# Kernel optimization log

Measured on AMD Instinct MI355X. Metric: run time of the kernel, lower is better.

The kernel has to match this reference:

```python
import jax, jax.numpy as jnp
import numpy as np
import math

D_MODEL = 1024
N_HEADS = 16
HEAD_DIM = D_MODEL // N_HEADS
N_LEVELS = 4
B = 8
MAX_LEN = 1024
LN_EPS = 1e-5


def setup_inputs() -> dict:
    key = jax.random.key(0)
    ks = jax.random.split(key, 6)
    lengths = np.array([1024, 768, 512, 896, 640, 1024, 576, 704], dtype=np.int32)
    N = int(lengths.sum())  # 6144
    batch_offsets = jnp.asarray(np.concatenate([[0], np.cumsum(lengths)]).astype(np.int32))
    x = jax.random.normal(ks[0], (N, D_MODEL), jnp.float32)
    levels = jax.random.randint(ks[1], (N, 1), 0, N_LEVELS).astype(jnp.float32)
    coords = jax.random.uniform(ks[2], (N, 2), jnp.float32) * 64.0
    positions = jnp.concatenate([levels, coords], axis=-1)  # [N, 3] = (level, y, x)
    ln_gamma = jnp.ones((D_MODEL,), jnp.float32)
    ln_beta = jnp.zeros((D_MODEL,), jnp.float32)
    w_qkv = jax.random.normal(ks[3], (D_MODEL, 3 * D_MODEL), jnp.float32) / math.sqrt(D_MODEL)
    w_out = jax.random.normal(ks[4], (D_MODEL, D_MODEL), jnp.float32) / math.sqrt(D_MODEL)
    # learned per-level, per-head rotary frequencies for 2 spatial coords
    base = 10.0 ** (-2.0 * np.arange(HEAD_DIM // 2) / HEAD_DIM)  # rope_theta = 10.0
    rope_freqs = (jnp.asarray(base, jnp.float32)[None, None, :, None]
                  * (1.0 + 0.1 * jax.random.normal(ks[5], (N_LEVELS, N_HEADS, HEAD_DIM // 2, 2), jnp.float32)))
    return {"x": x, "positions": positions, "batch_offsets": batch_offsets,
            "ln_gamma": ln_gamma, "ln_beta": ln_beta, "w_qkv": w_qkv,
            "w_out": w_out, "rope_freqs": rope_freqs}


def _layernorm(x, g, b):
    mu = jnp.mean(x, axis=-1, keepdims=True)
    var = jnp.mean(jnp.square(x - mu), axis=-1, keepdims=True)
    return (x - mu) * jax.lax.rsqrt(var + LN_EPS) * g + b


def _forward(x, positions, batch_offsets, ln_gamma, ln_beta, w_qkv, w_out, rope_freqs):
    N = x.shape[0]
    residual = x
    h = _layernorm(x, ln_gamma, ln_beta)
    q, k, v = jnp.split(h @ w_qkv, 3, axis=-1)  # each [N, D]

    # ragged -> padded batch layout
    tok = jnp.arange(N)
    batch_ids = jnp.searchsorted(batch_offsets[1:], tok, side='right')  # [N]
    pos_in_seq = tok - batch_offsets[batch_ids]                         # [N]
    lengths = batch_offsets[1:] - batch_offsets[:-1]                    # [B]
    valid = jnp.arange(MAX_LEN)[None, :] < lengths[:, None]             # [B, L]

    def pad(t, fill=0.0):
        out = jnp.full((B, MAX_LEN) + t.shape[1:], fill, t.dtype)
        return out.at[batch_ids, pos_in_seq].set(t)

    qp = pad(q).reshape(B, MAX_LEN, N_HEADS, HEAD_DIM)
    kp = pad(k).reshape(B, MAX_LEN, N_HEADS, HEAD_DIM)
    vp = pad(v).reshape(B, MAX_LEN, N_HEADS, HEAD_DIM)
    posp = pad(positions, fill=1.0)  # padded positions filled with ones (as in torch code)

    # multilevel RoPE: per-level learned freqs over 2 spatial coords
    lvl = jnp.clip(posp[..., 0].astype(jnp.int32), 0, N_LEVELS - 1)  # [B, L]
    f = rope_freqs[lvl]                                              # [B, L, H, K, 2]
    ang = jnp.einsum('blhkc,blc->blhk', f, posp[..., 1:])            # [B, L, H, K]
    cos, sin = jnp.cos(ang), jnp.sin(ang)

    def rot(t):  # rotate consecutive pairs of head_dim
        t = t.reshape(B, MAX_LEN, N_HEADS, HEAD_DIM // 2, 2)
        a, b = t[..., 0], t[..., 1]
        return jnp.stack([a * cos - b * sin, a * sin + b * cos], axis=-1).reshape(
            B, MAX_LEN, N_HEADS, HEAD_DIM)

    qr, kr = rot(qp), rot(kp)

    # masked SDPA (padded keys excluded; padded query rows are dropped on un-pad)
    scale = 1.0 / math.sqrt(HEAD_DIM)
    scores = jnp.einsum('blhd,bmhd->bhlm', qr, kr) * scale
    scores = jnp.where(valid[:, None, None, :], scores, jnp.float32(-1e9))
    attn = jax.nn.softmax(scores, axis=-1)
    o = jnp.einsum('bhlm,bmhd->blhd', attn, vp).reshape(B, MAX_LEN, D_MODEL)

    o = o[batch_ids, pos_in_seq]  # back to packed [N, D]
    return o @ w_out + residual


def reference(x, positions, batch_offsets, ln_gamma, ln_beta, w_qkv, w_out, rope_freqs):
    return _forward(x, positions, batch_offsets, ln_gamma, ln_beta, w_qkv, w_out, rope_freqs)
```

## Files before the change

### kernel.cpp

```cpp
#include <hip/hip_runtime.h>


typedef float  f32x4  __attribute__((ext_vector_type(4)));
typedef __bf16 bf16x8 __attribute__((ext_vector_type(8)));
typedef __bf16 bf16x4 __attribute__((ext_vector_type(4)));
typedef short  s16x4  __attribute__((ext_vector_type(4)));
typedef short  s16x8  __attribute__((ext_vector_type(8)));
typedef unsigned short u16x4 __attribute__((ext_vector_type(4)));

typedef __attribute__((address_space(1))) void as1_void_t;
typedef __attribute__((address_space(3))) void as3_void_t;

static __device__ __forceinline__ unsigned short f2bf(float f) {
  unsigned int u = __float_as_uint(f);
  u += 0x7fffu + ((u >> 16) & 1u);
  return (unsigned short)(u >> 16);
}
static __device__ __forceinline__ float bf2f(unsigned short s) {
  return __uint_as_float(((unsigned int)s) << 16);
}

static __device__ __forceinline__ void gload_lds16(const void* g, void* l) {
  __builtin_amdgcn_global_load_lds((as1_void_t*)g, (as3_void_t*)l, 16, 0, 0);
}

static __device__ __forceinline__ f32x4 mfma32(bf16x8 a, bf16x8 b, f32x4 c) {
  return __builtin_amdgcn_mfma_f32_16x16x32_bf16(a, b, c, 0, 0, 0);
}
static __device__ __forceinline__ f32x4 mfma16(s16x4 a, s16x4 b, f32x4 c) {
  return __builtin_amdgcn_mfma_f32_16x16x16bf16_1k(a, b, c, 0, 0, 0);
}

__global__ __launch_bounds__(256) void ln_kernel(
    const float* __restrict__ x, const float* __restrict__ gamma,
    const float* __restrict__ beta, unsigned short* __restrict__ h, int Ntok) {
  int row  = blockIdx.x * 4 + (threadIdx.x >> 6);
  int lane = threadIdx.x & 63;
  const float* xr = x + (size_t)row * 1024;
  f32x4 v[4];
  float s = 0.f, ss = 0.f;
#pragma unroll
  for (int c = 0; c < 4; ++c) {
    v[c] = *(const f32x4*)(xr + c * 256 + lane * 4);
#pragma unroll
    for (int j = 0; j < 4; ++j) { s += v[c][j]; ss += v[c][j] * v[c][j]; }
  }
#pragma unroll
  for (int d = 1; d < 64; d <<= 1) {
    s  += __shfl_xor(s, d);
    ss += __shfl_xor(ss, d);
  }
  float mu  = s * (1.f / 1024.f);
  float var = ss * (1.f / 1024.f) - mu * mu;
  float inv = rsqrtf(var + 1e-5f);
#pragma unroll
  for (int c = 0; c < 4; ++c) {
    f32x4 gv = *(const f32x4*)(gamma + c * 256 + lane * 4);
    f32x4 bv = *(const f32x4*)(beta  + c * 256 + lane * 4);
    u16x4 hv;
#pragma unroll
    for (int j = 0; j < 4; ++j) hv[j] = f2bf((v[c][j] - mu) * inv * gv[j] + bv[j]);
    *(u16x4*)(h + (size_t)row * 1024 + c * 256 + lane * 4) = hv;
  }
}

__global__ __launch_bounds__(256) void transpose_bf16(
    const float* __restrict__ in, unsigned short* __restrict__ out, int R, int C) {
  __shared__ unsigned short tile[64][65];
  int c0 = blockIdx.x * 64, r0 = blockIdx.y * 64;
  int t = threadIdx.x;
  int tr = t >> 6, tc = t & 63;
#pragma unroll
  for (int i = 0; i < 16; ++i) {
    int rr = i * 4 + tr;
    tile[tc][rr] = f2bf(in[(size_t)(r0 + rr) * C + c0 + tc]);
  }
  __syncthreads();
#pragma unroll
  for (int i = 0; i < 16; ++i) {
    int cc = i * 4 + tr;
    out[(size_t)(c0 + cc) * R + r0 + tc] = tile[cc][tc];
  }
}

__global__ __launch_bounds__(256) void gemm_qkv(
    const unsigned short* __restrict__ A, const unsigned short* __restrict__ Bt,
    unsigned short* __restrict__ Cqkv, int M, int K) {
  __shared__ unsigned short Alds[128 * 32];
  __shared__ unsigned short Blds[128 * 32];
  int n0 = blockIdx.x * 128, m0 = blockIdx.y * 128;
  int t = threadIdx.x, lane = t & 63, wave = t >> 6;
  int wr = wave >> 1, wc = wave & 1;
  int r = lane & 15, g = lane >> 4;
  f32x4 acc[4][4] = {};

  int srow = lane >> 2;
  int scol = (lane & 3) * 8;

  for (int k0 = 0; k0 < K; k0 += 32) {
    __syncthreads();
#pragma unroll
    for (int c = 0; c < 2; ++c) {
      int seg = wave * 2 + c;
      gload_lds16(A  + (size_t)(m0 + seg * 16 + srow) * K + k0 + scol,
                  Alds + seg * 16 * 32);
      gload_lds16(Bt + (size_t)(n0 + seg * 16 + srow) * K + k0 + scol,
                  Blds + seg * 16 * 32);
    }
    __syncthreads();
    bf16x8 a[4], b[4];
#pragma unroll
    for (int m = 0; m < 4; ++m)
      a[m] = *(const bf16x8*)(Alds + (wr * 64 + m * 16 + r) * 32 + g * 8);
#pragma unroll
    for (int n = 0; n < 4; ++n)
      b[n] = *(const bf16x8*)(Blds + (wc * 64 + n * 16 + r) * 32 + g * 8);
#pragma unroll
    for (int m = 0; m < 4; ++m)
#pragma unroll
      for (int n = 0; n < 4; ++n)
        acc[m][n] = mfma32(a[m], b[n], acc[m][n]);
  }

#pragma unroll
  for (int mi = 0; mi < 4; ++mi) {
    int grow0 = m0 + wr * 64 + mi * 16 + g * 4;
#pragma unroll
    for (int ni = 0; ni < 4; ++ni) {
      int gcol = n0 + wc * 64 + ni * 16 + r;
      f32x4 v = acc[mi][ni];
#pragma unroll
      for (int e = 0; e < 4; ++e) {
        int which = gcol >> 10, rem = gcol & 1023, hh = rem >> 6, d = rem & 63;
        Cqkv[((size_t)(which * 16 + hh) * M + grow0 + e) * 64 + d] = f2bf(v[e]);
      }
    }
  }
}

__global__ __launch_bounds__(256) void gemm_out64(
    const unsigned short* __restrict__ A, const unsigned short* __restrict__ Bt,
    const float* __restrict__ residual, float* __restrict__ Cf,
    int M, int Ncols, int K) {
  __shared__ unsigned short Alds[64 * 32];
  __shared__ unsigned short Blds[128 * 32];
  int n0 = blockIdx.x * 128, m0 = blockIdx.y * 64;
  int t = threadIdx.x, lane = t & 63, wave = t >> 6;
  int wr = wave >> 1, wc = wave & 1;
  int r = lane & 15, g = lane >> 4;
  f32x4 acc[2][4] = {};

  int srow = lane >> 2;
  int scol = (lane & 3) * 8;

  for (int k0 = 0; k0 < K; k0 += 32) {
    __syncthreads();
    gload_lds16(A + (size_t)(m0 + wave * 16 + srow) * K + k0 + scol,
                Alds + wave * 16 * 32);
#pragma unroll
    for (int c = 0; c < 2; ++c) {
      int seg = wave * 2 + c;
      gload_lds16(Bt + (size_t)(n0 + seg * 16 + srow) * K + k0 + scol,
                  Blds + seg * 16 * 32);
    }
    __syncthreads();
    bf16x8 a[2], b[4];
#pragma unroll
    for (int m = 0; m < 2; ++m)
      a[m] = *(const bf16x8*)(Alds + (wr * 32 + m * 16 + r) * 32 + g * 8);
#pragma unroll
    for (int n = 0; n < 4; ++n)
      b[n] = *(const bf16x8*)(Blds + (wc * 64 + n * 16 + r) * 32 + g * 8);
#pragma unroll
    for (int m = 0; m < 2; ++m)
#pragma unroll
      for (int n = 0; n < 4; ++n)
        acc[m][n] = mfma32(a[m], b[n], acc[m][n]);
  }

#pragma unroll
  for (int mi = 0; mi < 2; ++mi) {
    int grow0 = m0 + wr * 32 + mi * 16 + g * 4;
#pragma unroll
    for (int ni = 0; ni < 4; ++ni) {
      int gcol = n0 + wc * 64 + ni * 16 + r;
      f32x4 v = acc[mi][ni];
#pragma unroll
      for (int e = 0; e < 4; ++e)
        Cf[(size_t)(grow0 + e) * Ncols + gcol] =
            v[e] + residual[(size_t)(grow0 + e) * Ncols + gcol];
    }
  }
}

__global__ __launch_bounds__(256) void rope_kernel(
    unsigned short* __restrict__ QKV, const float* __restrict__ pos,
    const float* __restrict__ freqs, int Ntok) {
  int t = blockIdx.x * 256 + threadIdx.x;
  if (t >= Ntok * 512) return;
  int kk = t & 31, h = (t >> 5) & 15, i = t >> 9;
  float lvlf = pos[i * 3 + 0];
  float py   = pos[i * 3 + 1];
  float px   = pos[i * 3 + 2];
  int lvl = (int)lvlf;
  lvl = lvl < 0 ? 0 : (lvl > 3 ? 3 : lvl);
  const float* fp = freqs + (((lvl * 16 + h) * 32 + kk) << 1);
  float ang = fp[0] * py + fp[1] * px;
  float s, c;
  __sincosf(ang, &s, &c);
  size_t qoff = ((size_t)h * Ntok + i) * 64 + 2 * kk;
  size_t koff = qoff + (size_t)16 * Ntok * 64;
  unsigned int q2 = *(const unsigned int*)(QKV + qoff);
  float qa = bf2f((unsigned short)(q2 & 0xffff));
  float qb = bf2f((unsigned short)(q2 >> 16));
  *(unsigned int*)(QKV + qoff) =
      (unsigned int)f2bf(qa * c - qb * s) | ((unsigned int)f2bf(qa * s + qb * c) << 16);
  unsigned int k2 = *(const unsigned int*)(QKV + koff);
  float ka = bf2f((unsigned short)(k2 & 0xffff));
  float kb = bf2f((unsigned short)(k2 >> 16));
  *(unsigned int*)(QKV + koff) =
      (unsigned int)f2bf(ka * c - kb * s) | ((unsigned int)f2bf(ka * s + kb * c) << 16);
}

__global__ __launch_bounds__(256) void vtrans_kernel(
    const unsigned short* __restrict__ Vp, unsigned short* __restrict__ VtG,
    int Ntok) {
  __shared__ unsigned short tile[64][72];
  int blk = blockIdx.x;
  int h = blk & 15, t0 = (blk >> 4) * 64;
  int t = threadIdx.x;
  {
    int tok = t >> 2, dc = (t & 3) * 16;
    const unsigned short* src = Vp + ((size_t)h * Ntok + t0 + tok) * 64 + dc;
    *(s16x8*)&tile[tok][dc]     = *(const s16x8*)src;
    *(s16x8*)&tile[tok][dc + 8] = *(const s16x8*)(src + 8);
  }
  __syncthreads();
  {
    int d = t >> 2, tc = (t & 3) * 16;
    s16x8 o0, o1;
#pragma unroll
    for (int j = 0; j < 8; ++j) {
      o0[j] = (short)tile[tc + j][d];
      o1[j] = (short)tile[tc + 8 + j][d];
    }
    unsigned short* dst = VtG + (size_t)(h * 64 + d) * Ntok + t0 + tc;
    *(s16x8*)dst       = o0;
    *(s16x8*)(dst + 8) = o1;
  }
}

__global__ __launch_bounds__(256, 4) void attn_kernel(
    const unsigned short* __restrict__ QKV,
    const unsigned short* __restrict__ VtG, const int* __restrict__ boff,
    unsigned short* __restrict__ O, int Ntok) {
  __shared__ unsigned short Klds[64][72];
  __shared__ unsigned short Vt[64][72];
  const float SCALE_LOG2 = 0.125f * 1.44269504088896340736f;
  const s16x4 ones16 = {(short)0x3F80, (short)0x3F80, (short)0x3F80, (short)0x3F80};

  int bid = blockIdx.x;
  int x = bid & 7, idx = bid >> 3;
  int nq[8];
#pragma unroll
  for (int bb = 0; bb < 8; ++bb) nq[bb] = (boff[bb + 1] - boff[bb]) >> 6;
  int j = 0, rem = idx;
  for (int it = 0; it < 16; ++it) {
    int c = 0;
#pragma unroll
    for (int bb = 0; bb < 8; ++bb) c += (nq[bb] > j) ? 2 : 0;
    if (rem < c) break;
    rem -= c; ++j;
  }
  int k = 0;
  {
    int c2 = 0;
#pragma unroll
    for (int kk = 0; kk < 16; ++kk)
      if (nq[kk >> 1] > j) { if (c2 == rem) k = kk; ++c2; }
  }
  int h = (x + 8 * k) & 15, b = k >> 1, qblk = j;
  int off = boff[b], len = boff[b + 1] - off;
  int q0 = qblk * 64;
  if (q0 >= len) return;

  int t = threadIdx.x, lane = t & 63, wave = t >> 6;
  int r = lane & 15, g4 = lane >> 4;
  const unsigned short* Qg = QKV + (size_t)h * Ntok * 64;
  const unsigned short* Kg = QKV + (size_t)(16 + h) * Ntok * 64;
  int qmax = off + len - 1;

  bf16x8 qf[2];
  {
    int qtok = off + q0 + wave * 16 + r;
    if (qtok > qmax) qtok = qmax;
#pragma unroll
    for (int c = 0; c < 2; ++c)
      qf[c] = *(const bf16x8*)(Qg + (size_t)qtok * 64 + c * 32 + g4 * 8);
  }

  float m = -1e30f;
  f32x4 o[4] = {};
  f32x4 o_sum = {};

  int srow = t >> 2, sseg = t & 3;
  const unsigned short* Vrow = VtG + (size_t)(h * 64 + srow) * Ntok;

  s16x8 kr[2], vr[2];
  {
    int ktok = off + srow; if (ktok > qmax) ktok = qmax;
#pragma unroll
    for (int c = 0; c < 2; ++c)
      kr[c] = *(const s16x8*)(Kg + (size_t)ktok * 64 + sseg * 16 + c * 8);
#pragma unroll
    for (int c = 0; c < 2; ++c) {
      int tc = sseg * 16 + c * 8; if (tc + 8 > len) tc = len - 8;
      vr[c] = *(const s16x8*)(Vrow + off + tc);
    }
  }

  for (int kt = 0; kt < len; kt += 64) {
    asm volatile("s_waitcnt lgkmcnt(0)" ::: "memory");
    __builtin_amdgcn_s_barrier();
    __builtin_amdgcn_sched_barrier(0);
#pragma unroll
    for (int c = 0; c < 2; ++c) {
      *(s16x8*)&Klds[srow][sseg * 16 + c * 8] = kr[c];
      *(s16x8*)&Vt[srow][sseg * 16 + c * 8]   = vr[c];
    }
    int ktn = kt + 64;
    if (ktn < len) {
      int ktok = off + ktn + srow; if (ktok > qmax) ktok = qmax;
#pragma unroll
      for (int c = 0; c < 2; ++c)
        kr[c] = *(const s16x8*)(Kg + (size_t)ktok * 64 + sseg * 16 + c * 8);
#pragma unroll
      for (int c = 0; c < 2; ++c) {
        int tc = ktn + sseg * 16 + c * 8; if (tc + 8 > len) tc = len - 8;
        vr[c] = *(const s16x8*)(Vrow + off + tc);
      }
    }
    asm volatile("s_waitcnt lgkmcnt(0)" ::: "memory");
    __builtin_amdgcn_s_barrier();
    __builtin_amdgcn_sched_barrier(0);

    f32x4 s[4];
    __builtin_amdgcn_s_setprio(1);
#pragma unroll
    for (int sub = 0; sub < 4; ++sub) {
      bf16x8 ka0 = *(const bf16x8*)(&Klds[sub * 16 + r][g4 * 8]);
      bf16x8 ka1 = *(const bf16x8*)(&Klds[sub * 16 + r][32 + g4 * 8]);
      f32x4 acc = {};
      acc = mfma32(ka0, qf[0], acc);
      acc = mfma32(ka1, qf[1], acc);
      s[sub] = acc;
    }
    __builtin_amdgcn_s_setprio(0);

    bool tail = (kt + 64 > len);
    s16x4 pf[4];
    {
      float sc[4][4];
      float ms[4];
#pragma unroll
      for (int sub = 0; sub < 4; ++sub) {
#pragma unroll
        for (int e = 0; e < 4; ++e) {
          float v = s[sub][e];
          if (tail && (kt + sub * 16 + 4 * g4 + e >= len)) v = -1e30f;
          sc[sub][e] = v;
        }
        ms[sub] = fmaxf(fmaxf(sc[sub][0], sc[sub][1]),
                        fmaxf(sc[sub][2], sc[sub][3]));
      }
      float tmax = fmaxf(fmaxf(ms[0], ms[1]), fmaxf(ms[2], ms[3]));
      if (!__all(tmax * SCALE_LOG2 <= m + 8.f)) {
        float tm = tmax * SCALE_LOG2;
        tm = fmaxf(tm, __shfl_xor(tm, 16));
        tm = fmaxf(tm, __shfl_xor(tm, 32));
        float mnew = fmaxf(m, tm);
        float alpha = exp2f(m - mnew);
        m = mnew;
#pragma unroll
        for (int e = 0; e < 4; ++e) o_sum[e] *= alpha;
#pragma unroll
        for (int dt = 0; dt < 4; ++dt)
#pragma unroll
          for (int e = 0; e < 4; ++e) o[dt][e] *= alpha;
      }
#pragma unroll
      for (int sub = 0; sub < 4; ++sub) {
        bf16x4 pb;
#pragma unroll
        for (int e = 0; e < 4; ++e)
          pb[e] = (__bf16)exp2f(fmaf(sc[sub][e], SCALE_LOG2, -m));
        pf[sub] = __builtin_bit_cast(s16x4, pb);
      }
    }

    __builtin_amdgcn_s_setprio(1);
#pragma unroll
    for (int sub = 0; sub < 4; ++sub)
      o_sum = mfma16(pf[sub], ones16, o_sum);
#pragma unroll
    for (int dt = 0; dt < 4; ++dt)
#pragma unroll
      for (int sub = 0; sub < 4; ++sub) {
        s16x4 vf = *(const s16x4*)(&Vt[dt * 16 + r][sub * 16 + 4 * g4]);
        o[dt] = mfma16(pf[sub], vf, o[dt]);
      }
    __builtin_amdgcn_s_setprio(0);
  }

  {
    float il[4];
#pragma unroll
    for (int e = 0; e < 4; ++e) il[e] = 1.0f / o_sum[e];
#pragma unroll
    for (int dt = 0; dt < 4; ++dt)
#pragma unroll
      for (int e = 0; e < 4; ++e) {
        int tl = q0 + wave * 16 + 4 * g4 + e;
        if (tl < len)
          O[(size_t)(off + tl) * 1024 + h * 64 + dt * 16 + r] =
              f2bf(o[dt][e] * il[e]);
      }
  }
}

extern "C" void kernel_launch(void* const* d_in, const int* in_sizes, int n_in,
                              void* d_out, int out_size, void* d_ws, size_t ws_size,
                              hipStream_t stream) {
  const float* x     = (const float*)d_in[0];
  const float* pos   = (const float*)d_in[1];
  const int*   boff  = (const int*)d_in[2];
  const float* gamma = (const float*)d_in[3];
  const float* beta  = (const float*)d_in[4];
  const float* wqkv  = (const float*)d_in[5];
  const float* wout  = (const float*)d_in[6];
  const float* freqs = (const float*)d_in[7];
  float* out = (float*)d_out;
  int N  = in_sizes[0] / 1024;
  int Bn = in_sizes[2] - 1;

  char* ws = (char*)d_ws;
  unsigned short* wqkvT = (unsigned short*)ws;
  unsigned short* woutT = (unsigned short*)(ws + (size_t)3072 * 1024 * 2);
  unsigned short* QKV   = (unsigned short*)(ws + (size_t)3072 * 1024 * 2 +
                                            (size_t)1024 * 1024 * 2);
  size_t qkvBytes = (size_t)48 * N * 64 * 2;
  unsigned short* hbuf = (unsigned short*)((char*)QKV + qkvBytes);
  unsigned short* VtG  = hbuf;
  unsigned short* Vp   = QKV + (size_t)32 * N * 64;
  unsigned short* Obuf = Vp;

  ln_kernel<<<N / 4, 256, 0, stream>>>(x, gamma, beta, hbuf, N);
  transpose_bf16<<<dim3(3072 / 64, 1024 / 64), 256, 0, stream>>>(wqkv, wqkvT, 1024, 3072);
  transpose_bf16<<<dim3(1024 / 64, 1024 / 64), 256, 0, stream>>>(wout, woutT, 1024, 1024);
  gemm_qkv<<<dim3(3072 / 128, N / 128), 256, 0, stream>>>(
      hbuf, wqkvT, QKV, N, 1024);
  rope_kernel<<<(N * 512) / 256, 256, 0, stream>>>(QKV, pos, freqs, N);
  vtrans_kernel<<<16 * (N / 64), 256, 0, stream>>>(Vp, VtG, N);
  attn_kernel<<<16 * (N / 64), 256, 0, stream>>>(QKV, VtG, boff, Obuf, N);
  gemm_out64<<<dim3(1024 / 128, N / 64), 256, 0, stream>>>(
      Obuf, woutT, x, out, N, 1024, 1024);
}
```

Baseline: 188.8 us.

## Widen QKV GEMM K-step to 64 and simplify attention block mapping

The QKV GEMM now stages two 32-wide K slices per iteration into doubled LDS buffers, which halves the number of barrier pairs per K loop while raising LDS use per block. The attention kernel drops its ragged block-index decoding loop and uses a fixed grid of 8*16*16 blocks, mapping directly to (query block, head, batch). Blocks whose query tile is past the sequence end exit early. The price is launching idle blocks, and the loss of the length-sorted ordering that scheduled long sequences first.

```diff
diff --git a/kernel.cpp b/kernel.cpp
--- a/kernel.cpp
+++ b/kernel.cpp
@@ -86,8 +86,8 @@
 __global__ __launch_bounds__(256) void gemm_qkv(
     const unsigned short* __restrict__ A, const unsigned short* __restrict__ Bt,
     unsigned short* __restrict__ Cqkv, int M, int K) {
-  __shared__ unsigned short Alds[128 * 32];
-  __shared__ unsigned short Blds[128 * 32];
+  __shared__ unsigned short Alds[2][128 * 32];
+  __shared__ unsigned short Blds[2][128 * 32];
   int n0 = blockIdx.x * 128, m0 = blockIdx.y * 128;
   int t = threadIdx.x, lane = t & 63, wave = t >> 6;
   int wr = wave >> 1, wc = wave & 1;
@@ -97,29 +97,34 @@
   int srow = lane >> 2;
   int scol = (lane & 3) * 8;
 
-  for (int k0 = 0; k0 < K; k0 += 32) {
+  for (int k0 = 0; k0 < K; k0 += 64) {
     __syncthreads();
 #pragma unroll
-    for (int c = 0; c < 2; ++c) {
-      int seg = wave * 2 + c;
-      gload_lds16(A  + (size_t)(m0 + seg * 16 + srow) * K + k0 + scol,
-                  Alds + seg * 16 * 32);
-      gload_lds16(Bt + (size_t)(n0 + seg * 16 + srow) * K + k0 + scol,
-                  Blds + seg * 16 * 32);
-    }
+    for (int half = 0; half < 2; ++half)
+#pragma unroll
+      for (int c = 0; c < 2; ++c) {
+        int seg = wave * 2 + c;
+        gload_lds16(A  + (size_t)(m0 + seg * 16 + srow) * K + k0 + half * 32 + scol,
+                    Alds[half] + seg * 16 * 32);
+        gload_lds16(Bt + (size_t)(n0 + seg * 16 + srow) * K + k0 + half * 32 + scol,
+                    Blds[half] + seg * 16 * 32);
+      }
     __syncthreads();
-    bf16x8 a[4], b[4];
-#pragma unroll
-    for (int m = 0; m < 4; ++m)
-      a[m] = *(const bf16x8*)(Alds + (wr * 64 + m * 16 + r) * 32 + g * 8);
-#pragma unroll
-    for (int n = 0; n < 4; ++n)
-      b[n] = *(const bf16x8*)(Blds + (wc * 64 + n * 16 + r) * 32 + g * 8);
-#pragma unroll
-    for (int m = 0; m < 4; ++m)
+#pragma unroll
+    for (int half = 0; half < 2; ++half) {
+      bf16x8 a[4], b[4];
+#pragma unroll
+      for (int m = 0; m < 4; ++m)
+        a[m] = *(const bf16x8*)(Alds[half] + (wr * 64 + m * 16 + r) * 32 + g * 8);
 #pragma unroll
       for (int n = 0; n < 4; ++n)
-        acc[m][n] = mfma32(a[m], b[n], acc[m][n]);
+        b[n] = *(const bf16x8*)(Blds[half] + (wc * 64 + n * 16 + r) * 32 + g * 8);
+#pragma unroll
+      for (int m = 0; m < 4; ++m)
+#pragma unroll
+        for (int n = 0; n < 4; ++n)
+          acc[m][n] = mfma32(a[m], b[n], acc[m][n]);
+    }
   }
 
 #pragma unroll
@@ -260,30 +265,13 @@
   const s16x4 ones16 = {(short)0x3F80, (short)0x3F80, (short)0x3F80, (short)0x3F80};
 
   int bid = blockIdx.x;
-  int x = bid & 7, idx = bid >> 3;
-  int nq[8];
-#pragma unroll
-  for (int bb = 0; bb < 8; ++bb) nq[bb] = (boff[bb + 1] - boff[bb]) >> 6;
-  int j = 0, rem = idx;
-  for (int it = 0; it < 16; ++it) {
-    int c = 0;
-#pragma unroll
-    for (int bb = 0; bb < 8; ++bb) c += (nq[bb] > j) ? 2 : 0;
-    if (rem < c) break;
-    rem -= c; ++j;
-  }
-  int k = 0;
-  {
-    int c2 = 0;
-#pragma unroll
-    for (int kk = 0; kk < 16; ++kk)
-      if (nq[kk >> 1] > j) { if (c2 == rem) k = kk; ++c2; }
-  }
-  int h = (x + 8 * k) & 15, b = k >> 1, qblk = j;
+  int x = bid & 7, i = bid >> 3;
+  int qblk = i & 15;
+  int p = x + 8 * (i >> 4);
+  int h = p & 15, b = p >> 4;
   int off = boff[b], len = boff[b + 1] - off;
   int q0 = qblk * 64;
   if (q0 >= len) return;
-
   int t = threadIdx.x, lane = t & 63, wave = t >> 6;
   int r = lane & 15, g4 = lane >> 4;
   const unsigned short* Qg = QKV + (size_t)h * Ntok * 64;
@@ -461,7 +449,7 @@
       hbuf, wqkvT, QKV, N, 1024);
   rope_kernel<<<(N * 512) / 256, 256, 0, stream>>>(QKV, pos, freqs, N);
   vtrans_kernel<<<16 * (N / 64), 256, 0, stream>>>(Vp, VtG, N);
-  attn_kernel<<<16 * (N / 64), 256, 0, stream>>>(QKV, VtG, boff, Obuf, N);
+  attn_kernel<<<8 * 16 * 16, 256, 0, stream>>>(QKV, VtG, boff, Obuf, N);
   gemm_out64<<<dim3(1024 / 128, N / 64), 256, 0, stream>>>(
       Obuf, woutT, x, out, N, 1024, 1024);
 }
```

New measurement: 177.7 us. 1.06x faster.
